# Performance work log

Measured on AMD Instinct MI355X. Metric: run time of the kernel, lower is better.

## Reference

```python
import jax, jax.numpy as jnp
import numpy as np

D_MODEL = 128
HEADS = 8
D_K = D_MODEL // HEADS  # 16


def setup_inputs() -> dict:
    key = jax.random.key(0)
    k1, k2, k3, k4, k5 = jax.random.split(key, 5)
    B, S = 8, 2048
    x = jax.random.normal(k1, (B, S, D_MODEL), dtype=jnp.float32)
    # torch nn.Linear weights: y = x @ W.T, shape [out, in]
    scale = 1.0 / np.sqrt(D_MODEL)
    W_k = jax.random.normal(k2, (D_MODEL, D_MODEL), dtype=jnp.float32) * scale
    W_q = jax.random.normal(k3, (D_MODEL, D_MODEL), dtype=jnp.float32) * scale
    W_v = jax.random.normal(k4, (D_MODEL, D_MODEL), dtype=jnp.float32) * scale
    W_o = jax.random.normal(k5, (D_MODEL, D_MODEL), dtype=jnp.float32) * scale
    return {"x": x, "W_k": W_k, "W_q": W_q, "W_v": W_v, "W_o": W_o}


def reference(x, W_k, W_q, W_v, W_o):
    # Faithful to source: Q, K, V are ALL computed with W_k (source bug),
    # W_q / W_v are unused parameters.
    B, S, D = x.shape
    kqv = x @ W_k.T  # [B, S, D]; serves as key, query and value
    h = kqv.reshape(B, S, HEADS, D_K).transpose(0, 2, 1, 3)  # [B, H, S, d_k]
    scores = jnp.einsum("bhqd,bhkd->bhqk", h, h) / jnp.sqrt(jnp.float32(D_K))
    attn = jax.nn.softmax(scores, axis=-1)  # [B, H, S, S]
    ctx = jnp.einsum("bhqk,bhkd->bhqd", attn, h)  # [B, H, S, d_k]
    ctx = ctx.transpose(0, 2, 1, 3).reshape(B, S, D)
    return ctx @ W_o.T
```

## Files before the change

### kernel.cpp

```cpp
#include <hip/hip_runtime.h>

#define Bc 8
#define Sc 2048
#define Dc 128
#define Hc 8
#define DKc 16
#define NROW (Bc*Sc)

template <int MODE>
__global__ __launch_bounds__(256) void proj_kernel(const float* __restrict__ x,
                                                   const float* __restrict__ W,
                                                   float* __restrict__ out) {
    __shared__ float xs[64 * 128];
    const int blk = blockIdx.x;
    const int t = threadIdx.x;

    const float4* x4 = (const float4*)(x + (size_t)blk * 64 * 128);
    float4* xs4 = (float4*)xs;
#pragma unroll
    for (int i = 0; i < 8; ++i) xs4[t + 256 * i] = x4[t + 256 * i];
    __syncthreads();

    const int tr = t >> 4;
    const int tc = t & 15;

    float acc[4][8];
#pragma unroll
    for (int r = 0; r < 4; ++r)
#pragma unroll
        for (int j = 0; j < 8; ++j) acc[r][j] = 0.0f;

    const float4* W4 = (const float4*)W;
#pragma unroll 2
    for (int k4 = 0; k4 < 32; ++k4) {
        float4 xv[4];
#pragma unroll
        for (int r = 0; r < 4; ++r) xv[r] = xs4[(tr * 4 + r) * 32 + k4];
#pragma unroll
        for (int j = 0; j < 8; ++j) {
            const float4 wv = W4[(tc * 8 + j) * 32 + k4];
#pragma unroll
            for (int r = 0; r < 4; ++r) {
                acc[r][j] = fmaf(xv[r].x, wv.x, acc[r][j]);
                acc[r][j] = fmaf(xv[r].y, wv.y, acc[r][j]);
                acc[r][j] = fmaf(xv[r].z, wv.z, acc[r][j]);
                acc[r][j] = fmaf(xv[r].w, wv.w, acc[r][j]);
            }
        }
    }

    const int row0 = blk * 64 + tr * 4;
#pragma unroll
    for (int r = 0; r < 4; ++r) {
        const int row = row0 + r;
        if (MODE == 0) {
            const int b = row >> 11;
            const int s = row & (Sc - 1);
#pragma unroll
            for (int j = 0; j < 8; ++j) {
                const int col = tc * 8 + j;
                const int hh = col >> 4;
                const int d = col & 15;
                out[(((size_t)(b * Hc + hh) * Sc) + s) * DKc + d] = acc[r][j];
            }
        } else {
#pragma unroll
            for (int j = 0; j < 8; ++j) out[(size_t)row * Dc + tc * 8 + j] = acc[r][j];
        }
    }
}

__global__ __launch_bounds__(256) void attn_kernel(const float* __restrict__ hws,
                                                   float* __restrict__ ctx) {
    const int bh = blockIdx.x >> 3;
    const int chunk = blockIdx.x & 7;
    const int q_idx = chunk * 256 + threadIdx.x;

    const float* Kb = hws + (size_t)bh * Sc * DKc;

    const float SCL = 0.25f * 1.44269504088896f;
    const float M2 = 16.0f * 1.44269504088896f;

    float q[16];
    {
        const float4* q4 = (const float4*)(Kb + (size_t)q_idx * DKc);
#pragma unroll
        for (int i = 0; i < 4; ++i) {
            const float4 v = q4[i];
            q[4 * i + 0] = v.x * SCL;
            q[4 * i + 1] = v.y * SCL;
            q[4 * i + 2] = v.z * SCL;
            q[4 * i + 3] = v.w * SCL;
        }
    }

    float acc[16];
#pragma unroll
    for (int j = 0; j < 16; ++j) acc[j] = 0.0f;
    float l = 0.0f;

#pragma unroll 2
    for (int t = 0; t < Sc; ++t) {
        const float4* kp4 = (const float4*)(Kb + (size_t)t * DKc);
        float4 kk[4];
        kk[0] = kp4[0]; kk[1] = kp4[1]; kk[2] = kp4[2]; kk[3] = kp4[3];
        const float* kv = (const float*)kk;

        float s = -M2;
#pragma unroll
        for (int j = 0; j < 16; ++j) s = fmaf(q[j], kv[j], s);
        const float p = __builtin_amdgcn_exp2f(s);
        l += p;
#pragma unroll
        for (int j = 0; j < 16; ++j) acc[j] = fmaf(p, kv[j], acc[j]);
    }

    const float inv = 1.0f / l;
    const int b = bh >> 3;
    const int hh = bh & 7;
    float4* op4 = (float4*)(ctx + ((size_t)(b * Sc + q_idx) * Dc) + hh * DKc);
#pragma unroll
    for (int i = 0; i < 4; ++i) {
        float4 v;
        v.x = acc[4 * i + 0] * inv;
        v.y = acc[4 * i + 1] * inv;
        v.z = acc[4 * i + 2] * inv;
        v.w = acc[4 * i + 3] * inv;
        op4[i] = v;
    }
}

extern "C" void kernel_launch(void* const* d_in, const int* in_sizes, int n_in,
                              void* d_out, int out_size, void* d_ws, size_t ws_size,
                              hipStream_t stream) {
    const float* x   = (const float*)d_in[0];
    const float* W_k = (const float*)d_in[1];
    const float* W_o = (const float*)d_in[4];
    float* out = (float*)d_out;

    float* h_ws   = (float*)d_ws;
    float* ctx_ws = h_ws + (size_t)NROW * Dc;

    proj_kernel<0><<<NROW / 64, 256, 0, stream>>>(x, W_k, h_ws);
    attn_kernel<<<Bc * Hc * 8, 256, 0, stream>>>(h_ws, ctx_ws);
    proj_kernel<1><<<NROW / 64, 256, 0, stream>>>(ctx_ws, W_o, out);
}
```

Before: 543.1 us.

## Stage K tiles in double-buffered LDS for attention; shrink projection row tile

The attention kernel now copies 128-key tiles of the head matrix into double-buffered shared memory, where the loop previously read the keys from global memory on every iteration. The score dot product is also split into four partial sums to shorten the FMA dependency chain. The projection kernels process 32 rows per block instead of 64, which doubles the grid size and cuts per-thread accumulators. The cost is a block-wide barrier per tile, and the projection blocks reuse each weight load across fewer rows.

```diff
diff --git a/kernel.cpp b/kernel.cpp
--- a/kernel.cpp
+++ b/kernel.cpp
@@ -11,47 +11,47 @@
 __global__ __launch_bounds__(256) void proj_kernel(const float* __restrict__ x,
                                                    const float* __restrict__ W,
                                                    float* __restrict__ out) {
-    __shared__ float xs[64 * 128];
+    __shared__ float xs[32 * 128];
     const int blk = blockIdx.x;
     const int t = threadIdx.x;
 
-    const float4* x4 = (const float4*)(x + (size_t)blk * 64 * 128);
+    const float4* x4 = (const float4*)(x + (size_t)blk * 32 * 128);
     float4* xs4 = (float4*)xs;
 #pragma unroll
-    for (int i = 0; i < 8; ++i) xs4[t + 256 * i] = x4[t + 256 * i];
+    for (int i = 0; i < 4; ++i) xs4[t + 256 * i] = x4[t + 256 * i];
     __syncthreads();
 
     const int tr = t >> 4;
     const int tc = t & 15;
 
-    float acc[4][8];
+    float acc[2][8];
 #pragma unroll
-    for (int r = 0; r < 4; ++r)
+    for (int r = 0; r < 2; ++r)
 #pragma unroll
         for (int j = 0; j < 8; ++j) acc[r][j] = 0.0f;
 
     const float4* W4 = (const float4*)W;
-#pragma unroll 2
+#pragma unroll 4
     for (int k4 = 0; k4 < 32; ++k4) {
-        float4 xv[4];
-#pragma unroll
-        for (int r = 0; r < 4; ++r) xv[r] = xs4[(tr * 4 + r) * 32 + k4];
+        const float4 xv0 = xs4[(tr * 2 + 0) * 32 + k4];
+        const float4 xv1 = xs4[(tr * 2 + 1) * 32 + k4];
 #pragma unroll
         for (int j = 0; j < 8; ++j) {
             const float4 wv = W4[(tc * 8 + j) * 32 + k4];
-#pragma unroll
-            for (int r = 0; r < 4; ++r) {
-                acc[r][j] = fmaf(xv[r].x, wv.x, acc[r][j]);
-                acc[r][j] = fmaf(xv[r].y, wv.y, acc[r][j]);
-                acc[r][j] = fmaf(xv[r].z, wv.z, acc[r][j]);
-                acc[r][j] = fmaf(xv[r].w, wv.w, acc[r][j]);
-            }
+            acc[0][j] = fmaf(xv0.x, wv.x, acc[0][j]);
+            acc[0][j] = fmaf(xv0.y, wv.y, acc[0][j]);
+            acc[0][j] = fmaf(xv0.z, wv.z, acc[0][j]);
+            acc[0][j] = fmaf(xv0.w, wv.w, acc[0][j]);
+            acc[1][j] = fmaf(xv1.x, wv.x, acc[1][j]);
+            acc[1][j] = fmaf(xv1.y, wv.y, acc[1][j]);
+            acc[1][j] = fmaf(xv1.z, wv.z, acc[1][j]);
+            acc[1][j] = fmaf(xv1.w, wv.w, acc[1][j]);
         }
     }
 
-    const int row0 = blk * 64 + tr * 4;
+    const int row0 = blk * 32 + tr * 2;
 #pragma unroll
-    for (int r = 0; r < 4; ++r) {
+    for (int r = 0; r < 2; ++r) {
         const int row = row0 + r;
         if (MODE == 0) {
             const int b = row >> 11;
@@ -70,8 +70,11 @@
     }
 }
 
+#define KT 128
+
 __global__ __launch_bounds__(256) void attn_kernel(const float* __restrict__ hws,
                                                    float* __restrict__ ctx) {
+    __shared__ float ks[2][KT * DKc];
     const int bh = blockIdx.x >> 3;
     const int chunk = blockIdx.x & 7;
     const int q_idx = chunk * 256 + threadIdx.x;
@@ -94,25 +97,59 @@
         }
     }
 
+    {
+        const float4* s0 = (const float4*)Kb;
+        float4* d0 = (float4*)ks[0];
+        d0[threadIdx.x] = s0[threadIdx.x];
+        d0[threadIdx.x + 256] = s0[threadIdx.x + 256];
+    }
+
     float acc[16];
 #pragma unroll
     for (int j = 0; j < 16; ++j) acc[j] = 0.0f;
     float l = 0.0f;
 
+    int cur = 0;
+    for (int tile = 0; tile < Sc / KT; ++tile) {
+        __syncthreads();
+        if (tile + 1 < Sc / KT) {
+            const float4* sn = (const float4*)(Kb + (size_t)(tile + 1) * KT * DKc);
+            float4* dn = (float4*)ks[cur ^ 1];
+            dn[threadIdx.x] = sn[threadIdx.x];
+            dn[threadIdx.x + 256] = sn[threadIdx.x + 256];
+        }
+        const float4* kb4 = (const float4*)ks[cur];
 #pragma unroll 2
-    for (int t = 0; t < Sc; ++t) {
-        const float4* kp4 = (const float4*)(Kb + (size_t)t * DKc);
-        float4 kk[4];
-        kk[0] = kp4[0]; kk[1] = kp4[1]; kk[2] = kp4[2]; kk[3] = kp4[3];
-        const float* kv = (const float*)kk;
-
-        float s = -M2;
-#pragma unroll
-        for (int j = 0; j < 16; ++j) s = fmaf(q[j], kv[j], s);
-        const float p = __builtin_amdgcn_exp2f(s);
-        l += p;
-#pragma unroll
-        for (int j = 0; j < 16; ++j) acc[j] = fmaf(p, kv[j], acc[j]);
+        for (int kk = 0; kk < KT; ++kk) {
+            const float4 k0 = kb4[kk * 4 + 0];
+            const float4 k1 = kb4[kk * 4 + 1];
+            const float4 k2 = kb4[kk * 4 + 2];
+            const float4 k3 = kb4[kk * 4 + 3];
+            float s0 = fmaf(q[0], k0.x, fmaf(q[1], k0.y, fmaf(q[2], k0.z, fmaf(q[3], k0.w, -M2))));
+            float s1 = fmaf(q[4], k1.x, fmaf(q[5], k1.y, fmaf(q[6], k1.z, q[7] * k1.w)));
+            float s2 = fmaf(q[8], k2.x, fmaf(q[9], k2.y, fmaf(q[10], k2.z, q[11] * k2.w)));
+            float s3 = fmaf(q[12], k3.x, fmaf(q[13], k3.y, fmaf(q[14], k3.z, q[15] * k3.w)));
+            const float s = (s0 + s1) + (s2 + s3);
+            const float p = __builtin_amdgcn_exp2f(s);
+            l += p;
+            acc[0]  = fmaf(p, k0.x, acc[0]);
+            acc[1]  = fmaf(p, k0.y, acc[1]);
+            acc[2]  = fmaf(p, k0.z, acc[2]);
+            acc[3]  = fmaf(p, k0.w, acc[3]);
+            acc[4]  = fmaf(p, k1.x, acc[4]);
+            acc[5]  = fmaf(p, k1.y, acc[5]);
+            acc[6]  = fmaf(p, k1.z, acc[6]);
+            acc[7]  = fmaf(p, k1.w, acc[7]);
+            acc[8]  = fmaf(p, k2.x, acc[8]);
+            acc[9]  = fmaf(p, k2.y, acc[9]);
+            acc[10] = fmaf(p, k2.z, acc[10]);
+            acc[11] = fmaf(p, k2.w, acc[11]);
+            acc[12] = fmaf(p, k3.x, acc[12]);
+            acc[13] = fmaf(p, k3.y, acc[13]);
+            acc[14] = fmaf(p, k3.z, acc[14]);
+            acc[15] = fmaf(p, k3.w, acc[15]);
+        }
+        cur ^= 1;
     }
 
     const float inv = 1.0f / l;
@@ -141,7 +178,7 @@
     float* h_ws   = (float*)d_ws;
     float* ctx_ws = h_ws + (size_t)NROW * Dc;
 
-    proj_kernel<0><<<NROW / 64, 256, 0, stream>>>(x, W_k, h_ws);
+    proj_kernel<0><<<NROW / 32, 256, 0, stream>>>(x, W_k, h_ws);
     attn_kernel<<<Bc * Hc * 8, 256, 0, stream>>>(h_ws, ctx_ws);
-    proj_kernel<1><<<NROW / 64, 256, 0, stream>>>(ctx_ws, W_o, out);
+    proj_kernel<1><<<NROW / 32, 256, 0, stream>>>(ctx_ws, W_o, out);
 }
```

After: 517.2 us. 4.8% less time.
